# Performance work log

Hardware: AMD Instinct MI355X
Metric: run time of the kernel (lower is better)

The kernel has to match this reference:

```python
import jax, jax.numpy as jnp
import numpy as np


def setup_inputs() -> dict:
    key = jax.random.key(0)
    k1, k2 = jax.random.split(key)
    N, P1, P2, D = 4, 8192, 8192, 3
    source_cloud = jax.random.normal(k1, (N, P1, D), dtype=jnp.float32)
    target_cloud = jax.random.normal(k2, (N, P2, D), dtype=jnp.float32)
    return {"source_cloud": source_cloud, "target_cloud": target_cloud}


def reference(source_cloud, target_cloud):
    # ChamferDistance.forward with defaults:
    #   bidirectional=False, reverse=False -> single-directional x->y
    #   point_reduction='sum', batch_reduction='mean', norm=2, no normals/weights
    x, y = source_cloud, target_cloud  # (N,P1,D), (N,P2,D)
    x2 = jnp.sum(x * x, axis=-1)                       # (N,P1)
    y2 = jnp.sum(y * y, axis=-1)                       # (N,P2)
    xy = jnp.einsum('npd,nqd->npq', x, y)              # (N,P1,P2)
    d2 = x2[:, :, None] + y2[None if False else slice(None), None, :] - 2.0 * xy  # (N,P1,P2)
    # squared L2 distances are non-negative; clamp tiny negatives from the GEMM trick
    nn_d2 = jnp.maximum(jnp.min(d2, axis=-1), 0.0)     # (N,P1) 1-NN squared dist
    per_cloud = jnp.sum(nn_d2, axis=1)                 # point_reduction='sum'
    loss = jnp.mean(per_cloud)                         # batch_reduction='mean'
    return loss
```

## Files before the change

### kernel.cpp

```cpp
#include <hip/hip_runtime.h>
#include <float.h>

#define N_BATCH 4
#define P1 8192
#define P2 8192
#define D 3

#define CHUNK 256
#define NCHUNK (P2 / CHUNK)
#define RSRC 8
#define TPB 256
#define SRC_PER_BLK (TPB * RSRC)
#define NSRCBLK (P1 / SRC_PER_BLK)
#define NMIN (N_BATCH * P1)

__global__ __launch_bounds__(TPB) void chamfer_main(
        const float* __restrict__ src,
        const float* __restrict__ tgt,
        float* __restrict__ ws) {
    const int bid = blockIdx.x;
    const int c   = bid % NCHUNK;
    const int sb  = (bid / NCHUNK) % NSRCBLK;
    const int n   = bid / (NCHUNK * NSRCBLK);
    const int t   = threadIdx.x;

    __shared__ float4 sT[CHUNK];

    {
        const int j = c * CHUNK + t;
        const float* p = tgt + ((size_t)n * P2 + j) * D;
        const float y0 = p[0], y1 = p[1], y2 = p[2];
        sT[t] = make_float4(-2.0f * y0, -2.0f * y1, -2.0f * y2,
                            y0 * y0 + y1 * y1 + y2 * y2);
    }
    __syncthreads();

    float x0[RSRC], x1[RSRC], x2[RSRC], m[RSRC];
#pragma unroll
    for (int i = 0; i < RSRC; ++i) {
        const int s = sb * SRC_PER_BLK + i * TPB + t;
        const float* p = src + ((size_t)n * P1 + s) * D;
        x0[i] = p[0]; x1[i] = p[1]; x2[i] = p[2];
        m[i] = FLT_MAX;
    }

#pragma unroll 2
    for (int j = 0; j < CHUNK; j += 2) {
        const float4 ya = sT[j];
        const float4 yb = sT[j + 1];
#pragma unroll
        for (int i = 0; i < RSRC; ++i) {
            float da = __builtin_fmaf(x0[i], ya.x, ya.w);
            da = __builtin_fmaf(x1[i], ya.y, da);
            da = __builtin_fmaf(x2[i], ya.z, da);
            float db = __builtin_fmaf(x0[i], yb.x, yb.w);
            db = __builtin_fmaf(x1[i], yb.y, db);
            db = __builtin_fmaf(x2[i], yb.z, db);
            m[i] = fminf(fminf(m[i], da), db);
        }
    }

#pragma unroll
    for (int i = 0; i < RSRC; ++i) {
        const int s = n * P1 + sb * SRC_PER_BLK + i * TPB + t;
        ws[(size_t)c * NMIN + s] = m[i];
    }
}

__global__ __launch_bounds__(TPB) void chamfer_reduce(
        const float* __restrict__ ws,
        const float* __restrict__ src,
        float* __restrict__ out) {
    const int gid = blockIdx.x * TPB + threadIdx.x;

    float v = ws[gid];
#pragma unroll
    for (int c = 1; c < NCHUNK; ++c)
        v = fminf(v, ws[(size_t)c * NMIN + gid]);

    const float* p = src + (size_t)gid * D;
    const float xs = p[0] * p[0] + p[1] * p[1] + p[2] * p[2];
    v = fmaxf(v + xs, 0.0f);

#pragma unroll
    for (int off = 32; off > 0; off >>= 1)
        v += __shfl_down(v, off, 64);
    __shared__ float sred[TPB / 64];
    const int lane = threadIdx.x & 63;
    const int w    = threadIdx.x >> 6;
    if (lane == 0) sred[w] = v;
    __syncthreads();
    if (threadIdx.x == 0) {
        float s = 0.0f;
#pragma unroll
        for (int i = 0; i < TPB / 64; ++i) s += sred[i];
        atomicAdd(out, s * (1.0f / N_BATCH));
    }
}

extern "C" void kernel_launch(void* const* d_in, const int* in_sizes, int n_in,
                              void* d_out, int out_size, void* d_ws, size_t ws_size,
                              hipStream_t stream) {
    const float* src = (const float*)d_in[0];
    const float* tgt = (const float*)d_in[1];
    float* out = (float*)d_out;
    float* ws  = (float*)d_ws;

    hipMemsetAsync(out, 0, sizeof(float), stream);

    const int nblocks = N_BATCH * NSRCBLK * NCHUNK;
    chamfer_main<<<nblocks, TPB, 0, stream>>>(src, tgt, ws);

    chamfer_reduce<<<NMIN / TPB, TPB, 0, stream>>>(ws, src, out);
}
```

Baseline: 37.80 us.

## Prepack target pairs for packed FMA and drop LDS staging

Adds a prepack kernel that writes target points in pairs, stored structure-of-arrays with the -2y terms and the squared norms. The main kernel then reads each pair with uniform global loads instead of staging through shared memory, and evaluates two distances at once with 2-wide vector FMAs, aiming for packed FP32 math. Tile sizes are also changed (CHUNK 256→128, RSRC 8→4) with an occupancy hint, and the output memset is folded into the prepack kernel. In exchange it adds an extra kernel launch, a larger workspace and doubles the min-reduction traffic across chunks.

```diff
diff --git a/kernel.cpp b/kernel.cpp
--- a/kernel.cpp
+++ b/kernel.cpp
@@ -1,68 +1,87 @@
 #include <hip/hip_runtime.h>
 #include <float.h>
+
+typedef float float2v __attribute__((ext_vector_type(2)));
+typedef float float4v __attribute__((ext_vector_type(4)));
 
 #define N_BATCH 4
 #define P1 8192
 #define P2 8192
 #define D 3
 
-#define CHUNK 256
+#define TPB 256
+#define RSRC 4
+#define CHUNK 128
 #define NCHUNK (P2 / CHUNK)
-#define RSRC 8
-#define TPB 256
+#define NPAIRG (CHUNK / 2)
+#define NMIN (N_BATCH * P1)
 #define SRC_PER_BLK (TPB * RSRC)
-#define NSRCBLK (P1 / SRC_PER_BLK)
-#define NMIN (N_BATCH * P1)
+#define NSB (NMIN / SRC_PER_BLK)
+#define NPK (N_BATCH * P2 / 2)
 
-__global__ __launch_bounds__(TPB) void chamfer_main(
+struct Pk8 { float v[8]; };
+
+__global__ __launch_bounds__(TPB) void chamfer_prepack(
+        const float* __restrict__ tgt, float* __restrict__ pk,
+        float* __restrict__ out) {
+    const int u = blockIdx.x * TPB + threadIdx.x;
+    if (u == 0) out[0] = 0.0f;
+    if (u >= NPK) return;
+    const int n = u >> 12;
+    const int q = u & 4095;
+    const float* pa = tgt + ((size_t)n * P2 + 2 * q) * D;
+    const float xa = pa[0], ya = pa[1], za = pa[2];
+    const float xb = pa[3], yb = pa[4], zb = pa[5];
+    float4v* o = (float4v*)(pk + (size_t)u * 8);
+    o[0] = (float4v){-2.0f * xa, -2.0f * xb, -2.0f * ya, -2.0f * yb};
+    o[1] = (float4v){-2.0f * za, -2.0f * zb,
+                     xa * xa + ya * ya + za * za,
+                     xb * xb + yb * yb + zb * zb};
+}
+
+__global__ __launch_bounds__(TPB, 6) void chamfer_main(
         const float* __restrict__ src,
-        const float* __restrict__ tgt,
+        const Pk8* __restrict__ pk,
         float* __restrict__ ws) {
     const int bid = blockIdx.x;
-    const int c   = bid % NCHUNK;
-    const int sb  = (bid / NCHUNK) % NSRCBLK;
-    const int n   = bid / (NCHUNK * NSRCBLK);
+    const int c   = bid & (NCHUNK - 1);
+    const int sb  = bid >> 6;
     const int t   = threadIdx.x;
+    const int n   = sb >> 3;
+    const int pkbase = n * 4096 + c * NPAIRG;
 
-    __shared__ float4 sT[CHUNK];
-
-    {
-        const int j = c * CHUNK + t;
-        const float* p = tgt + ((size_t)n * P2 + j) * D;
-        const float y0 = p[0], y1 = p[1], y2 = p[2];
-        sT[t] = make_float4(-2.0f * y0, -2.0f * y1, -2.0f * y2,
-                            y0 * y0 + y1 * y1 + y2 * y2);
-    }
-    __syncthreads();
-
-    float x0[RSRC], x1[RSRC], x2[RSRC], m[RSRC];
+    float2v bx0[RSRC], bx1[RSRC], bx2[RSRC];
+    float m[RSRC];
 #pragma unroll
     for (int i = 0; i < RSRC; ++i) {
         const int s = sb * SRC_PER_BLK + i * TPB + t;
-        const float* p = src + ((size_t)n * P1 + s) * D;
-        x0[i] = p[0]; x1[i] = p[1]; x2[i] = p[2];
+        const float* p = src + (size_t)s * D;
+        bx0[i] = (float2v){p[0], p[0]};
+        bx1[i] = (float2v){p[1], p[1]};
+        bx2[i] = (float2v){p[2], p[2]};
         m[i] = FLT_MAX;
     }
 
-#pragma unroll 2
-    for (int j = 0; j < CHUNK; j += 2) {
-        const float4 ya = sT[j];
-        const float4 yb = sT[j + 1];
+#pragma unroll 4
+    for (int q = 0; q < NPAIRG; ++q) {
+        const Pk8 P = pk[pkbase + q];
+        const float2v X = {P.v[0], P.v[1]};
+        const float2v Y = {P.v[2], P.v[3]};
+        const float2v Z = {P.v[4], P.v[5]};
+        const float2v W = {P.v[6], P.v[7]};
 #pragma unroll
         for (int i = 0; i < RSRC; ++i) {
-            float da = __builtin_fmaf(x0[i], ya.x, ya.w);
-            da = __builtin_fmaf(x1[i], ya.y, da);
-            da = __builtin_fmaf(x2[i], ya.z, da);
-            float db = __builtin_fmaf(x0[i], yb.x, yb.w);
-            db = __builtin_fmaf(x1[i], yb.y, db);
-            db = __builtin_fmaf(x2[i], yb.z, db);
-            m[i] = fminf(fminf(m[i], da), db);
+            float2v d;
+            d = __builtin_elementwise_fma(bx0[i], X, W);
+            d = __builtin_elementwise_fma(bx1[i], Y, d);
+            d = __builtin_elementwise_fma(bx2[i], Z, d);
+            m[i] = fminf(fminf(m[i], d.x), d.y);
         }
     }
 
 #pragma unroll
     for (int i = 0; i < RSRC; ++i) {
-        const int s = n * P1 + sb * SRC_PER_BLK + i * TPB + t;
+        const int s = sb * SRC_PER_BLK + i * TPB + t;
         ws[(size_t)c * NMIN + s] = m[i];
     }
 }
@@ -73,22 +92,22 @@
         float* __restrict__ out) {
     const int gid = blockIdx.x * TPB + threadIdx.x;
 
-    float v = ws[gid];
-#pragma unroll
+    float m = ws[gid];
+#pragma unroll 8
     for (int c = 1; c < NCHUNK; ++c)
-        v = fminf(v, ws[(size_t)c * NMIN + gid]);
+        m = fminf(m, ws[(size_t)c * NMIN + gid]);
 
     const float* p = src + (size_t)gid * D;
     const float xs = p[0] * p[0] + p[1] * p[1] + p[2] * p[2];
-    v = fmaxf(v + xs, 0.0f);
+    float r = fmaxf(m + xs, 0.0f);
 
 #pragma unroll
     for (int off = 32; off > 0; off >>= 1)
-        v += __shfl_down(v, off, 64);
+        r += __shfl_down(r, off, 64);
     __shared__ float sred[TPB / 64];
     const int lane = threadIdx.x & 63;
     const int w    = threadIdx.x >> 6;
-    if (lane == 0) sred[w] = v;
+    if (lane == 0) sred[w] = r;
     __syncthreads();
     if (threadIdx.x == 0) {
         float s = 0.0f;
@@ -104,12 +123,12 @@
     const float* src = (const float*)d_in[0];
     const float* tgt = (const float*)d_in[1];
     float* out = (float*)d_out;
-    float* ws  = (float*)d_ws;
+    float* pk  = (float*)d_ws;
+    float* ws  = pk + (size_t)NPK * 8;
 
-    hipMemsetAsync(out, 0, sizeof(float), stream);
+    chamfer_prepack<<<(NPK + TPB - 1) / TPB, TPB, 0, stream>>>(tgt, pk, out);
 
-    const int nblocks = N_BATCH * NSRCBLK * NCHUNK;
-    chamfer_main<<<nblocks, TPB, 0, stream>>>(src, tgt, ws);
+    chamfer_main<<<NSB * NCHUNK, TPB, 0, stream>>>(src, (const Pk8*)pk, ws);
 
     chamfer_reduce<<<NMIN / TPB, TPB, 0, stream>>>(ws, src, out);
 }
```

Measured after the change: 48.09 us. +27.2%, slower.
